# Kernel tuning notes

Hardware: AMD Instinct MI355X
Metric: run time of the kernel (lower is better)

## Reference

```python
import jax, jax.numpy as jnp
import numpy as np
from jax import lax

B, T = 8, 256
GRID = (8, 8, 8)
X, Y, Z = GRID
N = X * Y * Z            # 512 nodes
C_IN = C_OUT = 8         # 4096 / 512
R = 8                    # num_rand


def _stencil_mask():
    # 7-point stencil mask at kernel center (1,1,1)
    m = np.zeros((3, 3, 3), dtype=np.float32)
    c = 1
    m[c, c, c] = 1.0
    m[c - 1, c, c] = 1.0
    m[c + 1, c, c] = 1.0
    m[c, c - 1, c] = 1.0
    m[c, c + 1, c] = 1.0
    m[c, c, c - 1] = 1.0
    m[c, c, c + 1] = 1.0
    return jnp.asarray(m)


def setup_inputs() -> dict:
    key = jax.random.key(0)
    k1, k2, k3, k4 = jax.random.split(key, 4)
    x = jax.random.normal(k1, (B, T, C_IN * N), dtype=jnp.float32)
    # MaskedConv3d params (kernel 3x3x3)
    fan = C_IN * 27
    conv_w = jax.random.normal(k2, (C_OUT, C_IN, 3, 3, 3), dtype=jnp.float32) / np.sqrt(fan)
    conv_b = jnp.zeros((C_OUT,), dtype=jnp.float32)
    # RandomGraphMixer3D params (xavier-uniform-like)
    bound = np.sqrt(6.0 / (C_IN * R + C_OUT))
    mix_w = jax.random.uniform(k3, (C_OUT, C_IN, R), jnp.float32, -bound, bound)
    mix_b = jnp.zeros((C_OUT,), dtype=jnp.float32)
    rand_indices = jax.random.randint(k4, (N, R), 0, N, dtype=jnp.int32)
    alpha = jnp.float32(0.5)
    return {"x": x, "conv_w": conv_w, "conv_b": conv_b,
            "mix_w": mix_w, "mix_b": mix_b, "alpha": alpha,
            "rand_indices": rand_indices}


def reference(x, conv_w, conv_b, mix_w, mix_b, alpha, rand_indices):
    Bd, Td, D = x.shape
    xt = x.reshape(Bd * Td, C_IN, X, Y, Z)
    # --- masked 7-point stencil conv3d ---
    w = conv_w * _stencil_mask()  # broadcast over (O, I)
    y_local = lax.conv_general_dilated(
        xt, w, window_strides=(1, 1, 1), padding='SAME',
        dimension_numbers=('NCDHW', 'OIDHW', 'NCDHW'))
    y_local = y_local + conv_b[None, :, None, None, None]
    # --- random graph mixer: gather + contract ---
    x_nodes = xt.reshape(Bd * Td, C_IN, N)
    gathered = x_nodes[:, :, rand_indices]              # [BT, C, N, R]
    y_rand = jnp.einsum('ocr,bcnr->bon', mix_w, gathered) + mix_b[None, :, None]
    y_rand = y_rand.reshape(Bd * Td, C_OUT, X, Y, Z)
    # --- sigmoid blend ---
    a = jax.nn.sigmoid(alpha)
    yt = a * y_local + (1.0 - a) * y_rand
    return yt.reshape(Bd, Td, C_OUT * N)
```

## Files before the change

### kernel.cpp

```cpp
#include <hip/hip_runtime.h>
#include <math.h>

#define NNODES 512
#define CIN 8
#define COUT 8
#define RR 8
#define BTB 2
#define GUARD 64
#define SLOTS (GUARD + NNODES + GUARD)
#define SLAB_HW (SLOTS * 8)
#define LDS_HW (BTB * SLAB_HW)

typedef __attribute__((ext_vector_type(8))) short short8;
typedef __attribute__((ext_vector_type(4))) float floatx4;

__device__ __forceinline__ unsigned int pack_bf16(float a, float b) {
    unsigned int ua = __float_as_uint(a);
    unsigned int ub = __float_as_uint(b);
    ua = (ua + 0x7fffu + ((ua >> 16) & 1u)) >> 16;
    ub = (ub + 0x7fffu + ((ub >> 16) & 1u)) & 0xffff0000u;
    return ua | ub;
}

__global__ __launch_bounds__(256) void hybrid3d_v4(
    const float* __restrict__ x,
    const float* __restrict__ conv_w,
    const float* __restrict__ conv_b,
    const float* __restrict__ mix_w,
    const float* __restrict__ mix_b,
    const float* __restrict__ alpha_p,
    const int*   __restrict__ rand_idx,
    float* __restrict__ out)
{
    __shared__ unsigned short lds16[LDS_HW];
    float* wfold = (float*)lds16;

    const int tid  = threadIdx.x;
    const int wave = tid >> 6;
    const int lane = tid & 63;
    const int quad = lane >> 4;
    const int r16  = lane & 15;
    const int btl  = wave >> 1;
    const int half = wave & 1;

    const float a = 1.0f / (1.0f + expf(-alpha_p[0]));

    if (tid < 64) {
        const float* cw = conv_w + tid * 27;
        const float* mw = mix_w + tid * RR;
        float* wf = wfold + tid * 15;
        wf[0] = a * cw[13];
        wf[1] = a * cw[4];
        wf[2] = a * cw[22];
        wf[3] = a * cw[10];
        wf[4] = a * cw[16];
        wf[5] = a * cw[12];
        wf[6] = a * cw[14];
        const float oma = 1.0f - a;
#pragma unroll
        for (int r = 0; r < RR; ++r) wf[7 + r] = oma * mw[r];
    }
    const float bias = (r16 < 8) ? (a * conv_b[r16] + (1.0f - a) * mix_b[r16]) : 0.0f;
    __syncthreads();

    short8 bfrag[4];
#pragma unroll
    for (int i = 0; i < 4; ++i) {
        const int tap = 4 * i + quad;
        union { unsigned int u[4]; short8 s; } bf;
#pragma unroll
        for (int jp = 0; jp < 4; ++jp) {
            const int c0 = 2 * jp, c1 = 2 * jp + 1;
            float f0 = (r16 < 8 && tap < 15) ? wfold[(r16 * CIN + c0) * 15 + tap] : 0.0f;
            float f1 = (r16 < 8 && tap < 15) ? wfold[(r16 * CIN + c1) * 15 + tap] : 0.0f;
            bf.u[jp] = pack_bf16(f0, f1);
        }
        bfrag[i] = bf.s;
    }
    __syncthreads();

    {
        const int b = tid >> 7;
        const int s = tid & 127;
        const int slot = (s < GUARD) ? s : (NNODES + s);
        *(uint4*)&lds16[b * SLAB_HW + slot * 8] = make_uint4(0u, 0u, 0u, 0u);
    }
    const float* xg = x + ((size_t)blockIdx.x * BTB + btl) * (CIN * NNODES);
    unsigned short* slab = lds16 + btl * SLAB_HW;
#pragma unroll
    for (int j = 0; j < 4; ++j) {
        const int n = half * 256 + j * 64 + lane;
        float v[8];
#pragma unroll
        for (int c = 0; c < 8; ++c) v[c] = xg[c * NNODES + n];
        uint4 pk;
        pk.x = pack_bf16(v[0], v[1]);
        pk.y = pack_bf16(v[2], v[3]);
        pk.z = pack_bf16(v[4], v[5]);
        pk.w = pack_bf16(v[6], v[7]);
        *(uint4*)&slab[(GUARD + n) * 8] = pk;
    }
    __syncthreads();

    const char* slabp = (const char*)slab;
    float* outb = out + ((size_t)blockIdx.x * BTB + btl) * (COUT * NNODES);

    const int  rA   = (quad + 1) & 3;
    const bool q3f  = (quad == 3);
    const bool isq0 = (quad == 0);
    const int c0q = (quad == 0) ? 0 : (quad == 1) ? -1024 : (quad == 2) ? 1024 : -128;
    const int c1q = (quad == 0) ? 128 : (quad == 1) ? -16 : 16;
    const int w   = r16 & 7;
    const bool p1w = (quad == 1) ? (w > 0) : (quad == 2) ? (w < 7) : false;
    const int* rrow = rand_idx + rA;

#pragma unroll 2
    for (int tt = 0; tt < 16; ++tt) {
        const int t = half * 16 + tt;
        const int m = t * 16 + r16;
        const int hh = (m >> 3) & 7;
        const int base = 1024 + m * 16;

        const int gA = rrow[m * RR];
        const int gB = rrow[m * RR + 4];
        const int offA = 1024 + gA * 16;
        const int offB = 1024 + gB * 16;

        const bool p0 = (!q3f) || (hh > 0);
        const int off0 = p0 ? (base + c0q) : 0;
        const bool p1 = isq0 ? (hh < 7) : p1w;
        const int off1 = q3f ? offA : (p1 ? (base + c1q) : 0);
        const int off2 = q3f ? offB : offA;
        const int off3 = q3f ? 0 : offB;

        union { uint4 u; short8 s; } r0, r1, r2, r3;
        r0.u = *(const uint4*)(slabp + off0);
        r1.u = *(const uint4*)(slabp + off1);
        r2.u = *(const uint4*)(slabp + off2);
        r3.u = *(const uint4*)(slabp + off3);

        floatx4 acc_a = {bias, bias, bias, bias};
        floatx4 acc_b = {0.0f, 0.0f, 0.0f, 0.0f};
        acc_a = __builtin_amdgcn_mfma_f32_16x16x32_bf16(r0.s, bfrag[0], acc_a, 0, 0, 0);
        acc_b = __builtin_amdgcn_mfma_f32_16x16x32_bf16(r2.s, bfrag[2], acc_b, 0, 0, 0);
        acc_a = __builtin_amdgcn_mfma_f32_16x16x32_bf16(r1.s, bfrag[1], acc_a, 0, 0, 0);
        acc_b = __builtin_amdgcn_mfma_f32_16x16x32_bf16(r3.s, bfrag[3], acc_b, 0, 0, 0);

        if (r16 < 8) {
            float4 res;
            res.x = acc_a.x + acc_b.x;
            res.y = acc_a.y + acc_b.y;
            res.z = acc_a.z + acc_b.z;
            res.w = acc_a.w + acc_b.w;
            *(float4*)(outb + r16 * NNODES + t * 16 + quad * 4) = res;
        }
    }
}

extern "C" void kernel_launch(void* const* d_in, const int* in_sizes, int n_in,
                              void* d_out, int out_size, void* d_ws, size_t ws_size,
                              hipStream_t stream) {
    const float* x       = (const float*)d_in[0];
    const float* conv_w  = (const float*)d_in[1];
    const float* conv_b  = (const float*)d_in[2];
    const float* mix_w   = (const float*)d_in[3];
    const float* mix_b   = (const float*)d_in[4];
    const float* alpha_p = (const float*)d_in[5];
    const int*   rand_i  = (const int*)d_in[6];
    float* out = (float*)d_out;

    const int BT = in_sizes[0] / (CIN * NNODES);

    hybrid3d_v4<<<BT / BTB, 256, 0, stream>>>(x, conv_w, conv_b, mix_w, mix_b,
                                              alpha_p, rand_i, out);
}
```

Measured before the change: 106.0 us.

## Process one batch-time slice per block with compact LDS slab and prefetched indices

Each block now handles one BT slice instead of two, doubling the grid and shrinking LDS from two guarded slabs to a single slab with one zero slot. Out-of-range stencil neighbours go to that zero slot through explicit boundary predicates instead of guard regions. The folded weights are stored transposed so fragment loads use float2 reads. The random indices for the next tile are prefetched one iteration ahead. A launch-bounds occupancy hint is also added. Together these aim for higher occupancy and better latency hiding, at the cost of more blocks, repeated weight-folding setup per block, and extra predicate logic.

```diff
diff --git a/kernel.cpp b/kernel.cpp
--- a/kernel.cpp
+++ b/kernel.cpp
@@ -5,11 +5,7 @@
 #define CIN 8
 #define COUT 8
 #define RR 8
-#define BTB 2
-#define GUARD 64
-#define SLOTS (GUARD + NNODES + GUARD)
-#define SLAB_HW (SLOTS * 8)
-#define LDS_HW (BTB * SLAB_HW)
+#define SLAB_HW ((1 + NNODES) * 8 + 8)
 
 typedef __attribute__((ext_vector_type(8))) short short8;
 typedef __attribute__((ext_vector_type(4))) float floatx4;
@@ -22,7 +18,7 @@
     return ua | ub;
 }
 
-__global__ __launch_bounds__(256) void hybrid3d_v4(
+__global__ __launch_bounds__(256, 6) void hybrid3d_v5(
     const float* __restrict__ x,
     const float* __restrict__ conv_w,
     const float* __restrict__ conv_b,
@@ -32,7 +28,7 @@
     const int*   __restrict__ rand_idx,
     float* __restrict__ out)
 {
-    __shared__ unsigned short lds16[LDS_HW];
+    __shared__ unsigned short lds16[SLAB_HW];
     float* wfold = (float*)lds16;
 
     const int tid  = threadIdx.x;
@@ -40,25 +36,22 @@
     const int lane = tid & 63;
     const int quad = lane >> 4;
     const int r16  = lane & 15;
-    const int btl  = wave >> 1;
-    const int half = wave & 1;
 
     const float a = 1.0f / (1.0f + expf(-alpha_p[0]));
 
     if (tid < 64) {
         const float* cw = conv_w + tid * 27;
         const float* mw = mix_w + tid * RR;
-        float* wf = wfold + tid * 15;
-        wf[0] = a * cw[13];
-        wf[1] = a * cw[4];
-        wf[2] = a * cw[22];
-        wf[3] = a * cw[10];
-        wf[4] = a * cw[16];
-        wf[5] = a * cw[12];
-        wf[6] = a * cw[14];
         const float oma = 1.0f - a;
+        wfold[0 * 64 + tid] = a * cw[13];
+        wfold[1 * 64 + tid] = a * cw[4];
+        wfold[2 * 64 + tid] = a * cw[22];
+        wfold[3 * 64 + tid] = a * cw[10];
+        wfold[4 * 64 + tid] = a * cw[16];
+        wfold[5 * 64 + tid] = a * cw[12];
+        wfold[6 * 64 + tid] = a * cw[14];
 #pragma unroll
-        for (int r = 0; r < RR; ++r) wf[7 + r] = oma * mw[r];
+        for (int r = 0; r < RR; ++r) wfold[(7 + r) * 64 + tid] = oma * mw[r];
     }
     const float bias = (r16 < 8) ? (a * conv_b[r16] + (1.0f - a) * mix_b[r16]) : 0.0f;
     __syncthreads();
@@ -70,26 +63,22 @@
         union { unsigned int u[4]; short8 s; } bf;
 #pragma unroll
         for (int jp = 0; jp < 4; ++jp) {
-            const int c0 = 2 * jp, c1 = 2 * jp + 1;
-            float f0 = (r16 < 8 && tap < 15) ? wfold[(r16 * CIN + c0) * 15 + tap] : 0.0f;
-            float f1 = (r16 < 8 && tap < 15) ? wfold[(r16 * CIN + c1) * 15 + tap] : 0.0f;
+            float f0 = 0.0f, f1 = 0.0f;
+            if (r16 < 8 && tap < 15) {
+                const float2 f = *(const float2*)&wfold[tap * 64 + r16 * 8 + 2 * jp];
+                f0 = f.x; f1 = f.y;
+            }
             bf.u[jp] = pack_bf16(f0, f1);
         }
         bfrag[i] = bf.s;
     }
     __syncthreads();
 
-    {
-        const int b = tid >> 7;
-        const int s = tid & 127;
-        const int slot = (s < GUARD) ? s : (NNODES + s);
-        *(uint4*)&lds16[b * SLAB_HW + slot * 8] = make_uint4(0u, 0u, 0u, 0u);
-    }
-    const float* xg = x + ((size_t)blockIdx.x * BTB + btl) * (CIN * NNODES);
-    unsigned short* slab = lds16 + btl * SLAB_HW;
+    if (tid == 0) *(uint4*)&lds16[0] = make_uint4(0u, 0u, 0u, 0u);
+    const float* xg = x + (size_t)blockIdx.x * (CIN * NNODES);
 #pragma unroll
-    for (int j = 0; j < 4; ++j) {
-        const int n = half * 256 + j * 64 + lane;
+    for (int j = 0; j < 2; ++j) {
+        const int n = j * 256 + tid;
         float v[8];
 #pragma unroll
         for (int c = 0; c < 8; ++c) v[c] = xg[c * NNODES + n];
@@ -98,37 +87,46 @@
         pk.y = pack_bf16(v[2], v[3]);
         pk.z = pack_bf16(v[4], v[5]);
         pk.w = pack_bf16(v[6], v[7]);
-        *(uint4*)&slab[(GUARD + n) * 8] = pk;
+        *(uint4*)&lds16[(1 + n) * 8] = pk;
     }
     __syncthreads();
 
-    const char* slabp = (const char*)slab;
-    float* outb = out + ((size_t)blockIdx.x * BTB + btl) * (COUT * NNODES);
+    const char* slabp = (const char*)lds16;
+    float* outb = out + (size_t)blockIdx.x * (COUT * NNODES);
 
     const int  rA   = (quad + 1) & 3;
     const bool q3f  = (quad == 3);
     const bool isq0 = (quad == 0);
-    const int c0q = (quad == 0) ? 0 : (quad == 1) ? -1024 : (quad == 2) ? 1024 : -128;
-    const int c1q = (quad == 0) ? 128 : (quad == 1) ? -16 : 16;
+    const bool isq1 = (quad == 1);
+    const bool isq2 = (quad == 2);
+    const int c0q = isq0 ? 0 : isq1 ? -1024 : isq2 ? 1024 : -128;
+    const int c1q = isq0 ? 128 : isq1 ? -16 : 16;
     const int w   = r16 & 7;
-    const bool p1w = (quad == 1) ? (w > 0) : (quad == 2) ? (w < 7) : false;
+    const bool p1w = isq1 ? (w > 0) : (isq2 ? (w < 7) : false);
     const int* rrow = rand_idx + rA;
 
-#pragma unroll 2
-    for (int tt = 0; tt < 16; ++tt) {
-        const int t = half * 16 + tt;
+    const int t0 = wave * 8;
+    int gA = rrow[(t0 * 16 + r16) * RR];
+    int gB = rrow[(t0 * 16 + r16) * RR + 4];
+
+#pragma unroll 4
+    for (int tt = 0; tt < 8; ++tt) {
+        const int t = t0 + tt;
         const int m = t * 16 + r16;
+        const int base = 16 + m * 16;
         const int hh = (m >> 3) & 7;
-        const int base = 1024 + m * 16;
 
-        const int gA = rrow[m * RR];
-        const int gB = rrow[m * RR + 4];
-        const int offA = 1024 + gA * 16;
-        const int offB = 1024 + gB * 16;
+        const int curA = gA, curB = gB;
+        const int mn = (tt < 7) ? (m + 16) : m;
+        gA = rrow[mn * RR];
+        gB = rrow[mn * RR + 4];
 
-        const bool p0 = (!q3f) || (hh > 0);
+        const int offA = 16 + curA * 16;
+        const int offB = 16 + curB * 16;
+
+        const bool p0 = isq0 | (isq1 & (t >= 4)) | (isq2 & (t < 28)) | (q3f & (hh > 0));
+        const bool p1 = p1w | (isq0 & (hh < 7));
         const int off0 = p0 ? (base + c0q) : 0;
-        const bool p1 = isq0 ? (hh < 7) : p1w;
         const int off1 = q3f ? offA : (p1 ? (base + c1q) : 0);
         const int off2 = q3f ? offB : offA;
         const int off3 = q3f ? 0 : offB;
@@ -171,6 +169,6 @@
 
     const int BT = in_sizes[0] / (CIN * NNODES);
 
-    hybrid3d_v4<<<BT / BTB, 256, 0, stream>>>(x, conv_w, conv_b, mix_w, mix_b,
-                                              alpha_p, rand_i, out);
+    hybrid3d_v5<<<BT, 256, 0, stream>>>(x, conv_w, conv_b, mix_w, mix_b,
+                                        alpha_p, rand_i, out);
 }
```

New measurement: 105.9 us. About the same (-0.1%).
